# Kernel tuning notes

Hardware: AMD Instinct MI355X
Metric: run time of the kernel (lower is better)

The kernel has to match this reference:

```python
import jax, jax.numpy as jnp
import numpy as np
import math

D_MODEL = 1024
D_HEAD = 64
N_HEADS = D_MODEL // D_HEAD  # 16
COND = 768
EPS = 1e-6


def make_freqs():
    # AxialRoPE(dim=d_head//2, n_heads): freqs linspace in log-space, reshaped [dim//4, nh].T
    dim = D_HEAD // 2  # 32
    n = N_HEADS * dim // 4  # 128
    log_min = math.log(math.pi)
    log_max = math.log(10.0 * math.pi)
    freqs = jnp.exp(jnp.linspace(log_min, log_max, n + 1, dtype=jnp.float32)[:-1])
    return freqs.reshape(dim // 4, N_HEADS).T  # [n_heads, d_head//8] = [16, 8]


def setup_inputs() -> dict:
    key = jax.random.key(0)
    ks = jax.random.split(key, 6)
    N, H, W = 8, 32, 32
    x = jax.random.normal(ks[0], (N, H, W, D_MODEL), jnp.float32)
    pos = jax.random.uniform(ks[1], (N, H, W, 2), jnp.float32) * 2.0 - 1.0
    cond = jax.random.normal(ks[2], (N, COND), jnp.float32)
    norm_w = jax.random.normal(ks[3], (D_MODEL, COND), jnp.float32) * 0.02
    qkv_w = jax.random.normal(ks[4], (3 * D_MODEL, D_MODEL), jnp.float32) / math.sqrt(D_MODEL)
    out_w = jax.random.normal(ks[5], (D_MODEL, D_MODEL), jnp.float32) * 0.02
    scale = jnp.full((N_HEADS,), 10.0, jnp.float32)
    return {"x": x, "pos": pos, "cond": cond, "norm_w": norm_w,
            "qkv_w": qkv_w, "out_w": out_w, "scale": scale}


def rms_norm(x, scale, eps):
    mean_sq = jnp.mean(x * x, axis=-1, keepdims=True)
    return x * (scale * jax.lax.rsqrt(mean_sq + eps))


def apply_rotary(x, theta):
    # rotate first 2*d dims of the head; rest passes through
    d = theta.shape[-1]
    x1, x2, rest = x[..., :d], x[..., d:2 * d], x[..., 2 * d:]
    cos, sin = jnp.cos(theta), jnp.sin(theta)
    return jnp.concatenate([x1 * cos - x2 * sin, x2 * cos + x1 * sin, rest], axis=-1)


def reference(x, pos, cond, norm_w, qkv_w, out_w, scale):
    N, H, W, _ = x.shape
    S = H * W
    skip = x
    # AdaRMSNorm: scale = zero-init linear(cond) + 1
    ns = cond @ norm_w.T  # [N, d_model]
    xn = rms_norm(x, ns[:, None, None, :] + 1.0, EPS)
    # QKV projection, split 'n h w (t nh e)'
    qkv = (xn @ qkv_w.T).reshape(N, S, 3, N_HEADS, D_HEAD)
    q = jnp.transpose(qkv[:, :, 0], (0, 2, 1, 3))  # [N, nh, S, e]
    k = jnp.transpose(qkv[:, :, 1], (0, 2, 1, 3))
    v = jnp.transpose(qkv[:, :, 2], (0, 2, 1, 3))
    # cosine-sim scaling: per-head learned scale, L2-normalize q,k
    sqrt_scale = jnp.sqrt(scale)[:, None, None]  # [nh,1,1]
    q = q * (sqrt_scale * jax.lax.rsqrt(jnp.sum(q * q, -1, keepdims=True) + EPS))
    k = k * (sqrt_scale * jax.lax.rsqrt(jnp.sum(k * k, -1, keepdims=True) + EPS))
    # axial RoPE theta
    freqs = make_freqs()  # [nh, d_head//8]
    pos_f = pos.reshape(N, S, 2)
    theta_h = pos_f[:, :, None, 0:1] * freqs  # [N,S,nh,8]
    theta_w = pos_f[:, :, None, 1:2] * freqs
    theta = jnp.concatenate([theta_h, theta_w], axis=-1)  # [N,S,nh,16]
    theta = jnp.transpose(theta, (0, 2, 1, 3))  # [N,nh,S,16]
    q = apply_rotary(q, theta)
    k = apply_rotary(k, theta)
    # attention with scale=1.0 (cosine-sim already scaled)
    scores = jnp.einsum('bhqe,bhke->bhqk', q, k)
    probs = jax.nn.softmax(scores, axis=-1)
    o = jnp.einsum('bhqk,bhke->bhqe', probs, v)  # [N,nh,S,e]
    o = jnp.transpose(o, (0, 2, 1, 3)).reshape(N, H, W, D_MODEL)
    return o @ out_w.T + skip
```

## Files before the change

kernel.cpp:

```cpp
#include <hip/hip_runtime.h>
#include <hip/hip_bf16.h>
#include <math.h>

typedef __bf16 bf16;
typedef __bf16 bf16x8 __attribute__((ext_vector_type(8)));
typedef __bf16 bf16x4 __attribute__((ext_vector_type(4)));
typedef float f32x4 __attribute__((ext_vector_type(4)));
typedef float f32x16 __attribute__((ext_vector_type(16)));

#define MFMA16(a, b, c) __builtin_amdgcn_mfma_f32_16x16x32_bf16((a), (b), (c), 0, 0, 0)
#define MFMA32(a, b, c) __builtin_amdgcn_mfma_f32_32x32x16_bf16((a), (b), (c), 0, 0, 0)

__device__ __forceinline__ void gload_lds16(const void* g, void* l) {
  __builtin_amdgcn_global_load_lds((__attribute__((address_space(1))) void*)(g),
                                   (__attribute__((address_space(3))) void*)(l),
                                   16, 0, 0);
}

__global__ __launch_bounds__(256) void f2bf_kernel(const float* __restrict__ in0,
                                                   bf16* __restrict__ out0,
                                                   const float* __restrict__ in1,
                                                   bf16* __restrict__ out1, int n0) {
  int i = blockIdx.x * 256 + threadIdx.x;
  const float* in = (i < n0) ? in0 : in1;
  bf16* out = (i < n0) ? out0 : out1;
  int j = (i < n0) ? i : i - n0;
  float4 v = ((const float4*)in)[j];
  bf16x4 o;
  o[0] = (bf16)v.x; o[1] = (bf16)v.y; o[2] = (bf16)v.z; o[3] = (bf16)v.w;
  *(bf16x4*)(out + (size_t)j * 4) = o;
}

__global__ __launch_bounds__(256) void ns_kernel(const float* __restrict__ cond,
                                                 const float* __restrict__ norm_w,
                                                 float* __restrict__ nsp1) {
  int tid = blockIdx.x * 256 + threadIdx.x;
  int b = tid >> 10, c = tid & 1023;
  const float4* wv = (const float4*)(norm_w + (size_t)c * 768);
  const float4* cv = (const float4*)(cond + (size_t)b * 768);
  float acc = 0.f;
#pragma unroll 8
  for (int i = 0; i < 192; ++i) {
    float4 w4 = wv[i], c4 = cv[i];
    acc += w4.x * c4.x + w4.y * c4.y + w4.z * c4.z + w4.w * c4.w;
  }
  nsp1[tid] = acc + 1.0f;
}

__global__ __launch_bounds__(256) void rmsnorm_kernel(const float* __restrict__ x,
                                                      const float* __restrict__ nsp1,
                                                      bf16* __restrict__ xn) {
  int lane = threadIdx.x & 63, w = threadIdx.x >> 6;
  int m = blockIdx.x * 4 + w;
  int b = m >> 10;
  const float* xp = x + (size_t)m * 1024 + lane * 16;
  float v[16];
  float ss = 0.f;
#pragma unroll
  for (int i = 0; i < 4; ++i) {
    float4 t4 = ((const float4*)xp)[i];
    v[4 * i + 0] = t4.x; v[4 * i + 1] = t4.y; v[4 * i + 2] = t4.z; v[4 * i + 3] = t4.w;
    ss += t4.x * t4.x + t4.y * t4.y + t4.z * t4.z + t4.w * t4.w;
  }
#pragma unroll
  for (int off = 32; off >= 1; off >>= 1) ss += __shfl_xor(ss, off);
  float r = rsqrtf(ss * (1.0f / 1024.0f) + 1e-6f);
  const float* np = nsp1 + (size_t)b * 1024 + lane * 16;
  bf16x8 o0, o1;
#pragma unroll
  for (int j = 0; j < 8; ++j) o0[j] = (bf16)(v[j] * np[j] * r);
#pragma unroll
  for (int j = 0; j < 8; ++j) o1[j] = (bf16)(v[8 + j] * np[8 + j] * r);
  bf16* op = xn + (size_t)m * 1024 + lane * 16;
  *(bf16x8*)op = o0;
  *(bf16x8*)(op + 8) = o1;
}

template <int MODE>
__global__ __launch_bounds__(512, 2) void gemm256b(const bf16* __restrict__ A,
                                                   const bf16* __restrict__ B, int nbn,
                                                   bf16* __restrict__ qout, bf16* __restrict__ kout,
                                                   bf16* __restrict__ vtout, float* __restrict__ fout,
                                                   const float* __restrict__ skip,
                                                   const float* __restrict__ pos,
                                                   const float* __restrict__ scale) {
  constexpr int K = 1024;
  __shared__ __align__(16) bf16 sm[36864];
  const int t = threadIdx.x;
  const int cpx = gridDim.x >> 3;
  const int bid = blockIdx.x;
  const int virt = (bid & 7) * cpx + (bid >> 3);
  const int bn = virt % nbn, bm = virt / nbn;
  const int m0 = bm * 256, n0 = bn * 128;
  const int lane = t & 63, wid = t >> 6;
  const int wr = wid >> 1, wc = wid & 1;
  const int r16 = lane & 15, hi = lane >> 4;

  const int tq = t >> 3, c8 = t & 7, cp = c8 ^ (tq & 7);
  const size_t gA = (size_t)(m0 + tq * 2 + (cp >> 2)) * K + (cp & 3) * 8;
  const size_t gB = (size_t)(n0 + tq * 2 + (cp >> 2)) * K + (cp & 3) * 8;
  const size_t gj = (size_t)128 * K;
  const int ldst = t * 8;

  const int chunk = ((r16 & 1) * 4 + hi) ^ (r16 >> 1);
  int aoff[4], boff[4];
#pragma unroll
  for (int fr = 0; fr < 4; ++fr) aoff[fr] = (wr * 32 + fr * 8 + (r16 >> 1)) * 64 + chunk * 8;
#pragma unroll
  for (int fc = 0; fc < 4; ++fc)
    boff[fc] = (wc * 32 + fc * 8 + (r16 >> 1)) * 64 + chunk * 8 + 8192;

  f32x4 acc[4][4] = {};
  constexpr int NS = K >> 5;

#define STG(tile, slot)                                              \
  {                                                                  \
    const bf16* as_ = A + gA + (size_t)(tile) * 32;                  \
    const bf16* bs_ = B + gB + (size_t)(tile) * 32;                  \
    gload_lds16(as_, &sm[(slot) * 12288 + ldst]);                    \
    gload_lds16(as_ + gj, &sm[(slot) * 12288 + 4096 + ldst]);        \
    gload_lds16(bs_, &sm[(slot) * 12288 + 8192 + ldst]);             \
  }

  STG(0, 0);
  STG(1, 1);

  int sl = 0;
  int sl2 = 2;
  for (int s = 0; s < NS; ++s) {
    if (s < NS - 1) {
      asm volatile("s_waitcnt vmcnt(3)" ::: "memory");
    } else {
      asm volatile("s_waitcnt vmcnt(0)" ::: "memory");
    }
    __builtin_amdgcn_s_barrier();
    __builtin_amdgcn_sched_barrier(0);
    if (s + 2 < NS) STG(s + 2, sl2);
    bf16x8 af[4], bfr[4];
    const bf16* base = &sm[sl * 12288];
#pragma unroll
    for (int fr = 0; fr < 4; ++fr) af[fr] = *(const bf16x8*)&base[aoff[fr]];
#pragma unroll
    for (int fc = 0; fc < 4; ++fc) bfr[fc] = *(const bf16x8*)&base[boff[fc]];
    __builtin_amdgcn_s_setprio(1);
#pragma unroll
    for (int fc = 0; fc < 4; ++fc)
#pragma unroll
      for (int fr = 0; fr < 4; ++fr) acc[fr][fc] = MFMA16(af[fr], bfr[fc], acc[fr][fc]);
    __builtin_amdgcn_s_setprio(0);
    sl = (sl == 2) ? 0 : sl + 1;
    sl2 = (sl2 == 2) ? 0 : sl2 + 1;
  }
#undef STG

  if constexpr (MODE == 0) {
    const int p = n0 >> 10;
    if (p == 2) {
      const int hiq = ((hi & 1) << 1) | (hi >> 1);
#pragma unroll
      for (int fr = 0; fr < 4; ++fr) {
        int mrow = m0 + wr * 64 + fr * 16 + hiq * 4;
        int b = mrow >> 10, s0 = mrow & 1023;
#pragma unroll
        for (int fc = 0; fc < 4; ++fc) {
          int n = n0 + wc * 64 + fc * 16 + r16;
          int d = n & 63, hh = (n >> 6) & 15;
          bf16x4 pk;
          pk[0] = (bf16)acc[fr][fc][0]; pk[1] = (bf16)acc[fr][fc][1];
          pk[2] = (bf16)acc[fr][fc][2]; pk[3] = (bf16)acc[fr][fc][3];
          *(bf16x4*)&vtout[(((size_t)(b * 16 + hh) * 64 + d) << 10) + s0] = pk;
        }
      }
    } else {
      const int hh = ((n0 + wc * 64) >> 6) & 15;
      const float LOG2E = 1.4426950408889634f;
      const float sqv = sqrtf(scale[hh]) * (p == 0 ? LOG2E : 1.0f);
      const float f = __expf(1.14472988584940017f +
                             0.0179897502011134460f * (float)((r16 & 7) * 16 + hh));
      const bool is_h = (r16 < 8);
      bf16* dst = (p == 0) ? qout : kout;
#pragma unroll
      for (int fr = 0; fr < 4; ++fr) {
        int mrow = m0 + wr * 64 + fr * 16 + hi * 4;
        int b = mrow >> 10, s0 = mrow & 1023;
        float rr[4];
#pragma unroll
        for (int r = 0; r < 4; ++r) {
          float ss = acc[fr][0][r] * acc[fr][0][r] + acc[fr][1][r] * acc[fr][1][r] +
                     acc[fr][2][r] * acc[fr][2][r] + acc[fr][3][r] * acc[fr][3][r];
          ss += __shfl_xor(ss, 1);
          ss += __shfl_xor(ss, 2);
          ss += __shfl_xor(ss, 4);
          ss += __shfl_xor(ss, 8);
          rr[r] = sqv * rsqrtf(ss + 1e-6f);
        }
#pragma unroll
        for (int r = 0; r < 4; ++r) {
          float2 pp = *(const float2*)&pos[(((size_t)b << 10) + s0 + r) * 2];
          float th = (is_h ? pp.x : pp.y) * f;
          float sv, cv;
          __sincosf(th, &sv, &cv);
          float x1 = acc[fr][0][r] * rr[r];
          float x2 = acc[fr][1][r] * rr[r];
          size_t rowb = (((size_t)(b * 16 + hh) << 10) + s0 + r) * 64;
          dst[rowb + r16]      = (bf16)(x1 * cv - x2 * sv);
          dst[rowb + 16 + r16] = (bf16)(x2 * cv + x1 * sv);
          dst[rowb + 32 + r16] = (bf16)(acc[fr][2][r] * rr[r]);
          dst[rowb + 48 + r16] = (bf16)(acc[fr][3][r] * rr[r]);
        }
      }
    }
  } else {
#pragma unroll
    for (int fr = 0; fr < 4; ++fr) {
      int mrow = m0 + wr * 64 + fr * 16 + hi * 4;
#pragma unroll
      for (int fc = 0; fc < 4; ++fc) {
        int n = n0 + wc * 64 + fc * 16 + r16;
#pragma unroll
        for (int r = 0; r < 4; ++r) {
          size_t off = (size_t)(mrow + r) * 1024 + n;
          fout[off] = acc[fr][fc][r] + skip[off];
        }
      }
    }
  }
}

__global__ __launch_bounds__(256, 4) void attn_kernel(const bf16* __restrict__ q,
                                                      const bf16* __restrict__ k,
                                                      const bf16* __restrict__ vt,
                                                      bf16* __restrict__ o) {
  int bid = blockIdx.x;
  int virt = (bid & 7) * 128 + (bid >> 3);
  const int bh = virt >> 3;
  const int qt = virt & 7;
  const int b = bh >> 4, h = bh & 15;
  const int t = threadIdx.x, lane = t & 63, w = t >> 6;
  const int l31 = lane & 31, h2 = lane >> 5;

  __shared__ bf16 lK[2][4096];
  __shared__ bf16 lV[2][4096];

  const bf16* kp = k + (size_t)bh * 65536;
  const bf16* vp = vt + (size_t)bh * 65536;

  const bf16* qp = q + ((size_t)bh * 1024 + qt * 128 + w * 32) * 64;
  bf16x8 qf[4];
#pragma unroll
  for (int df = 0; df < 4; ++df)
    qf[df] = *(const bf16x8*)&qp[l31 * 64 + df * 16 + h2 * 8];

  bf16x8 ones;
#pragma unroll
  for (int i = 0; i < 8; ++i) ones[i] = (bf16)1.0f;

  const int srow0 = t >> 3, sc0 = t & 7;

  f32x16 oacc0 = {}, oacc1 = {}, lacc = {};

#define STGA(kt_, buf_)                                                            \
  {                                                                                \
    const bf16* kb_ = kp + (kt_) * 4096;                                           \
    const bf16* vb_ = vp + (kt_) * 64;                                             \
    _Pragma("unroll") for (int j = 0; j < 2; ++j) {                                \
      int row = srow0 + j * 32;                                                    \
      int se = ((sc0 ^ (row & 7)) << 3);                                           \
      gload_lds16(kb_ + (size_t)row * 64 + se, &lK[buf_][t * 8 + j * 2048]);       \
      gload_lds16(vb_ + (size_t)row * 1024 + se, &lV[buf_][t * 8 + j * 2048]);     \
    }                                                                              \
  }

  STGA(0, 0);
  STGA(1, 1);

  for (int kt = 0; kt < 16; ++kt) {
    const int cur = kt & 1;
    if (kt < 15) {
      asm volatile("s_waitcnt vmcnt(4)" ::: "memory");
    } else {
      asm volatile("s_waitcnt vmcnt(0)" ::: "memory");
    }
    __builtin_amdgcn_s_barrier();
    __builtin_amdgcn_sched_barrier(0);
    f32x16 sa0 = {}, sa1 = {};
    __builtin_amdgcn_s_setprio(1);
#pragma unroll
    for (int df = 0; df < 4; ++df) {
      int sw = l31 & 7;
      int ce = (((2 * df + h2) ^ sw) << 3);
      bf16x8 kf0 = *(const bf16x8*)&lK[cur][l31 * 64 + ce];
      bf16x8 kf1 = *(const bf16x8*)&lK[cur][(32 + l31) * 64 + ce];
      sa0 = MFMA32(kf0, qf[df], sa0);
      sa1 = MFMA32(kf1, qf[df], sa1);
    }
    __builtin_amdgcn_s_setprio(0);
    bf16x8 pa[4];
#pragma unroll
    for (int e = 0; e < 8; ++e) {
      pa[0][e] = (bf16)exp2f(sa0[e]);
      pa[1][e] = (bf16)exp2f(sa0[e + 8]);
      pa[2][e] = (bf16)exp2f(sa1[e]);
      pa[3][e] = (bf16)exp2f(sa1[e + 8]);
    }
    __builtin_amdgcn_s_setprio(1);
#pragma unroll
    for (int pk = 0; pk < 4; ++pk) {
      lacc = MFMA32(pa[pk], ones, lacc);
#pragma unroll
      for (int db = 0; db < 2; ++db) {
        int row = db * 32 + l31, sw = row & 7;
        bf16x8 vf = *(const bf16x8*)&lV[cur][row * 64 + (((2 * pk + h2) ^ sw) << 3)];
        if (db == 0) oacc0 = MFMA32(pa[pk], vf, oacc0);
        else         oacc1 = MFMA32(pa[pk], vf, oacc1);
      }
    }
    __builtin_amdgcn_s_setprio(0);
    __builtin_amdgcn_sched_barrier(0);
    __builtin_amdgcn_s_barrier();
    __builtin_amdgcn_sched_barrier(0);
    if (kt < 14) STGA(kt + 2, cur);
  }
#undef STGA

  f32x16 inv;
#pragma unroll
  for (int r = 0; r < 16; ++r) inv[r] = 1.f / lacc[r];
#pragma unroll
  for (int r = 0; r < 16; ++r) {
    int qrow = qt * 128 + w * 32 + (r & 3) + 8 * (r >> 2) + 4 * h2;
    size_t rowb = ((size_t)b * 1024 + qrow) * 1024 + h * 64;
    o[rowb + l31]      = (bf16)(oacc0[r] * inv[r]);
    o[rowb + 32 + l31] = (bf16)(oacc1[r] * inv[r]);
  }
}

extern "C" void kernel_launch(void* const* d_in, const int* in_sizes, int n_in,
                              void* d_out, int out_size, void* d_ws, size_t ws_size,
                              hipStream_t stream) {
  const float* x      = (const float*)d_in[0];
  const float* pos    = (const float*)d_in[1];
  const float* cond   = (const float*)d_in[2];
  const float* norm_w = (const float*)d_in[3];
  const float* qkv_w  = (const float*)d_in[4];
  const float* out_w  = (const float*)d_in[5];
  const float* scale  = (const float*)d_in[6];
  float* out = (float*)d_out;

  char* ws = (char*)d_ws;
  bf16* xn        = (bf16*)(ws + 0);
  bf16* qkv_w_bf  = (bf16*)(ws + 16777216);
  bf16* out_w_bf  = (bf16*)(ws + 23068672);
  float* nsp1     = (float*)(ws + 25165824);
  bf16* qraw      = (bf16*)(ws + 25198592);
  bf16* kraw      = (bf16*)(ws + 41975808);
  bf16* vt        = (bf16*)(ws + 58753024);
  bf16* o_attn    = xn;

  f2bf_kernel<<<4096, 256, 0, stream>>>(qkv_w, qkv_w_bf, out_w, out_w_bf, 786432);
  ns_kernel<<<32, 256, 0, stream>>>(cond, norm_w, nsp1);
  rmsnorm_kernel<<<2048, 256, 0, stream>>>(x, nsp1, xn);
  gemm256b<0><<<768, 512, 0, stream>>>(xn, qkv_w_bf, 24, qraw, kraw, vt, nullptr, nullptr,
                                       pos, scale);
  attn_kernel<<<1024, 256, 0, stream>>>(qraw, kraw, vt, o_attn);
  gemm256b<1><<<256, 512, 0, stream>>>(o_attn, out_w_bf, 8, nullptr, nullptr, nullptr, out, x,
                                       nullptr, nullptr);
}
```

Baseline: 187.0 us.

## Add dedicated QKV GEMM with K=64 tiles and split-phase load/MFMA pipeline

Replaces the templated QKV GEMM with a new kernel that stages 64-wide K tiles (16 iterations instead of 32) using a larger 3-slot LDS buffer. Each iteration is split into two phases, and the global-to-LDS loads for the next tile are interleaved between the MFMA halves with extra barriers. The aim is to halve the number of barrier and wait steps and to overlap memory traffic with compute. The larger shared memory footprint (about 144KB per block) may limit occupancy, and the extra barriers add synchronisation. The output projection GEMM becomes a non-templated kernel that keeps only its residual-add epilogue.

```diff
diff --git a/kernel.cpp b/kernel.cpp
--- a/kernel.cpp
+++ b/kernel.cpp
@@ -76,14 +76,180 @@
   *(bf16x8*)(op + 8) = o1;
 }
 
-template <int MODE>
+__global__ __launch_bounds__(512, 2) void gemm8p(const bf16* __restrict__ A,
+                                                 const bf16* __restrict__ B, int nbn,
+                                                 bf16* __restrict__ qout, bf16* __restrict__ kout,
+                                                 bf16* __restrict__ vtout,
+                                                 const float* __restrict__ pos,
+                                                 const float* __restrict__ scale) {
+  constexpr int K = 1024;
+  __shared__ __align__(16) bf16 sm[73728];
+  const int t = threadIdx.x;
+  const int cpx = gridDim.x >> 3;
+  const int bid = blockIdx.x;
+  const int virt = (bid & 7) * cpx + (bid >> 3);
+  const int bn = virt % nbn, bm = virt / nbn;
+  const int m0 = bm * 256, n0 = bn * 128;
+  const int lane = t & 63, wid = t >> 6;
+  const int wr = wid >> 1, wc = wid & 1;
+  const int r16 = lane & 15, hi = lane >> 4;
+  const int sw = r16 & 7;
+
+  const int row0 = t >> 3;
+  const int gc = (t & 7) ^ (row0 & 7);
+  const bf16* gAb = A + (size_t)(m0 + row0) * K + gc * 8;
+  const bf16* gBb = B + (size_t)(n0 + row0) * K + gc * 8;
+  const size_t rstep = (size_t)64 * K;
+  const int ldst = t * 8;
+
+  int aoff2[4][2], boff2[4][2];
+#pragma unroll
+  for (int fr = 0; fr < 4; ++fr)
+#pragma unroll
+    for (int ks = 0; ks < 2; ++ks) {
+      aoff2[fr][ks] = (wr * 64 + fr * 16 + r16) * 64 + (((ks * 4 + hi) ^ sw) << 3);
+      boff2[fr][ks] = 16384 + (wc * 64 + fr * 16 + r16) * 64 + (((ks * 4 + hi) ^ sw) << 3);
+    }
+
+  f32x4 acc[4][4] = {};
+
+#define STG2(tile_, slot_, pr_)                                                       \
+  {                                                                                   \
+    if ((pr_) < 2) {                                                                  \
+      gload_lds16(gAb + rstep * (2 * (pr_)) + (size_t)(tile_) * 64,                   \
+                  &sm[(slot_) * 24576 + (2 * (pr_)) * 4096 + ldst]);                  \
+      gload_lds16(gAb + rstep * (2 * (pr_) + 1) + (size_t)(tile_) * 64,               \
+                  &sm[(slot_) * 24576 + (2 * (pr_) + 1) * 4096 + ldst]);              \
+    } else {                                                                          \
+      gload_lds16(gBb + (size_t)(tile_) * 64, &sm[(slot_) * 24576 + 16384 + ldst]);   \
+      gload_lds16(gBb + rstep + (size_t)(tile_) * 64,                                 \
+                  &sm[(slot_) * 24576 + 20480 + ldst]);                               \
+    }                                                                                 \
+  }
+
+  STG2(0, 0, 0); STG2(0, 0, 1); STG2(0, 0, 2);
+  STG2(1, 1, 0); STG2(1, 1, 1); STG2(1, 1, 2);
+
+  int sl = 0, sl2 = 2;
+  for (int s = 0; s < 16; ++s) {
+    if (s < 15) {
+      asm volatile("s_waitcnt vmcnt(6)" ::: "memory");
+    } else {
+      asm volatile("s_waitcnt vmcnt(0)" ::: "memory");
+    }
+    __builtin_amdgcn_s_barrier();
+    __builtin_amdgcn_sched_barrier(0);
+    const bf16* base = &sm[sl * 24576];
+    const bool st = (s + 2 < 16);
+    bf16x8 ball[4][2], a2[2][2];
+#pragma unroll
+    for (int fc = 0; fc < 4; ++fc)
+#pragma unroll
+      for (int ks = 0; ks < 2; ++ks) ball[fc][ks] = *(const bf16x8*)&base[boff2[fc][ks]];
+#pragma unroll
+    for (int i = 0; i < 2; ++i)
+#pragma unroll
+      for (int ks = 0; ks < 2; ++ks) a2[i][ks] = *(const bf16x8*)&base[aoff2[i][ks]];
+    if (st) { STG2(s + 2, sl2, 0); STG2(s + 2, sl2, 1); }
+    asm volatile("s_waitcnt lgkmcnt(0)" ::: "memory");
+    __builtin_amdgcn_sched_barrier(0);
+    __builtin_amdgcn_s_setprio(1);
+#pragma unroll
+    for (int ks = 0; ks < 2; ++ks)
+#pragma unroll
+      for (int fc = 0; fc < 4; ++fc)
+#pragma unroll
+        for (int i = 0; i < 2; ++i)
+          acc[i][fc] = MFMA16(a2[i][ks], ball[fc][ks], acc[i][fc]);
+    __builtin_amdgcn_s_setprio(0);
+    __builtin_amdgcn_sched_barrier(0);
+    __builtin_amdgcn_s_barrier();
+    bf16x8 a3[2][2];
+#pragma unroll
+    for (int i = 0; i < 2; ++i)
+#pragma unroll
+      for (int ks = 0; ks < 2; ++ks) a3[i][ks] = *(const bf16x8*)&base[aoff2[2 + i][ks]];
+    if (st) STG2(s + 2, sl2, 2);
+    asm volatile("s_waitcnt lgkmcnt(0)" ::: "memory");
+    __builtin_amdgcn_sched_barrier(0);
+    __builtin_amdgcn_s_setprio(1);
+#pragma unroll
+    for (int ks = 0; ks < 2; ++ks)
+#pragma unroll
+      for (int fc = 0; fc < 4; ++fc)
+#pragma unroll
+        for (int i = 0; i < 2; ++i)
+          acc[2 + i][fc] = MFMA16(a3[i][ks], ball[fc][ks], acc[2 + i][fc]);
+    __builtin_amdgcn_s_setprio(0);
+    __builtin_amdgcn_sched_barrier(0);
+    __builtin_amdgcn_s_barrier();
+    sl = (sl == 2) ? 0 : sl + 1;
+    sl2 = (sl2 == 2) ? 0 : sl2 + 1;
+  }
+#undef STG2
+
+  const int p = n0 >> 10;
+  if (p == 2) {
+    const int hiq = ((hi & 1) << 1) | (hi >> 1);
+#pragma unroll
+    for (int fr = 0; fr < 4; ++fr) {
+      int mrow = m0 + wr * 64 + fr * 16 + hiq * 4;
+      int b = mrow >> 10, s0 = mrow & 1023;
+#pragma unroll
+      for (int fc = 0; fc < 4; ++fc) {
+        int n = n0 + wc * 64 + fc * 16 + r16;
+        int d = n & 63, hh = (n >> 6) & 15;
+        bf16x4 pk;
+        pk[0] = (bf16)acc[fr][fc][0]; pk[1] = (bf16)acc[fr][fc][1];
+        pk[2] = (bf16)acc[fr][fc][2]; pk[3] = (bf16)acc[fr][fc][3];
+        *(bf16x4*)&vtout[(((size_t)(b * 16 + hh) * 64 + d) << 10) + s0] = pk;
+      }
+    }
+  } else {
+    const int hh = ((n0 + wc * 64) >> 6) & 15;
+    const float LOG2E = 1.4426950408889634f;
+    const float sqv = sqrtf(scale[hh]) * (p == 0 ? LOG2E : 1.0f);
+    const float f = __expf(1.14472988584940017f +
+                           0.0179897502011134460f * (float)((r16 & 7) * 16 + hh));
+    const bool is_h = (r16 < 8);
+    bf16* dst = (p == 0) ? qout : kout;
+#pragma unroll
+    for (int fr = 0; fr < 4; ++fr) {
+      int mrow = m0 + wr * 64 + fr * 16 + hi * 4;
+      int b = mrow >> 10, s0 = mrow & 1023;
+      float rr[4];
+#pragma unroll
+      for (int r = 0; r < 4; ++r) {
+        float ss = acc[fr][0][r] * acc[fr][0][r] + acc[fr][1][r] * acc[fr][1][r] +
+                   acc[fr][2][r] * acc[fr][2][r] + acc[fr][3][r] * acc[fr][3][r];
+        ss += __shfl_xor(ss, 1);
+        ss += __shfl_xor(ss, 2);
+        ss += __shfl_xor(ss, 4);
+        ss += __shfl_xor(ss, 8);
+        rr[r] = sqv * rsqrtf(ss + 1e-6f);
+      }
+#pragma unroll
+      for (int r = 0; r < 4; ++r) {
+        float2 pp = *(const float2*)&pos[(((size_t)b << 10) + s0 + r) * 2];
+        float th = (is_h ? pp.x : pp.y) * f;
+        float sv, cv;
+        __sincosf(th, &sv, &cv);
+        float x1 = acc[fr][0][r] * rr[r];
+        float x2 = acc[fr][1][r] * rr[r];
+        size_t rowb = (((size_t)(b * 16 + hh) << 10) + s0 + r) * 64;
+        dst[rowb + r16]      = (bf16)(x1 * cv - x2 * sv);
+        dst[rowb + 16 + r16] = (bf16)(x2 * cv + x1 * sv);
+        dst[rowb + 32 + r16] = (bf16)(acc[fr][2][r] * rr[r]);
+        dst[rowb + 48 + r16] = (bf16)(acc[fr][3][r] * rr[r]);
+      }
+    }
+  }
+}
+
 __global__ __launch_bounds__(512, 2) void gemm256b(const bf16* __restrict__ A,
                                                    const bf16* __restrict__ B, int nbn,
-                                                   bf16* __restrict__ qout, bf16* __restrict__ kout,
-                                                   bf16* __restrict__ vtout, float* __restrict__ fout,
-                                                   const float* __restrict__ skip,
-                                                   const float* __restrict__ pos,
-                                                   const float* __restrict__ scale) {
+                                                   float* __restrict__ fout,
+                                                   const float* __restrict__ skip) {
   constexpr int K = 1024;
   __shared__ __align__(16) bf16 sm[36864];
   const int t = threadIdx.x;
@@ -125,8 +291,7 @@
   STG(0, 0);
   STG(1, 1);
 
-  int sl = 0;
-  int sl2 = 2;
+  int sl = 0, sl2 = 2;
   for (int s = 0; s < NS; ++s) {
     if (s < NS - 1) {
       asm volatile("s_waitcnt vmcnt(3)" ::: "memory");
@@ -153,75 +318,16 @@
   }
 #undef STG
 
-  if constexpr (MODE == 0) {
-    const int p = n0 >> 10;
-    if (p == 2) {
-      const int hiq = ((hi & 1) << 1) | (hi >> 1);
-#pragma unroll
-      for (int fr = 0; fr < 4; ++fr) {
-        int mrow = m0 + wr * 64 + fr * 16 + hiq * 4;
-        int b = mrow >> 10, s0 = mrow & 1023;
-#pragma unroll
-        for (int fc = 0; fc < 4; ++fc) {
-          int n = n0 + wc * 64 + fc * 16 + r16;
-          int d = n & 63, hh = (n >> 6) & 15;
-          bf16x4 pk;
-          pk[0] = (bf16)acc[fr][fc][0]; pk[1] = (bf16)acc[fr][fc][1];
-          pk[2] = (bf16)acc[fr][fc][2]; pk[3] = (bf16)acc[fr][fc][3];
-          *(bf16x4*)&vtout[(((size_t)(b * 16 + hh) * 64 + d) << 10) + s0] = pk;
-        }
-      }
-    } else {
-      const int hh = ((n0 + wc * 64) >> 6) & 15;
-      const float LOG2E = 1.4426950408889634f;
-      const float sqv = sqrtf(scale[hh]) * (p == 0 ? LOG2E : 1.0f);
-      const float f = __expf(1.14472988584940017f +
-                             0.0179897502011134460f * (float)((r16 & 7) * 16 + hh));
-      const bool is_h = (r16 < 8);
-      bf16* dst = (p == 0) ? qout : kout;
-#pragma unroll
-      for (int fr = 0; fr < 4; ++fr) {
-        int mrow = m0 + wr * 64 + fr * 16 + hi * 4;
-        int b = mrow >> 10, s0 = mrow & 1023;
-        float rr[4];
-#pragma unroll
-        for (int r = 0; r < 4; ++r) {
-          float ss = acc[fr][0][r] * acc[fr][0][r] + acc[fr][1][r] * acc[fr][1][r] +
-                     acc[fr][2][r] * acc[fr][2][r] + acc[fr][3][r] * acc[fr][3][r];
-          ss += __shfl_xor(ss, 1);
-          ss += __shfl_xor(ss, 2);
-          ss += __shfl_xor(ss, 4);
-          ss += __shfl_xor(ss, 8);
-          rr[r] = sqv * rsqrtf(ss + 1e-6f);
-        }
-#pragma unroll
-        for (int r = 0; r < 4; ++r) {
-          float2 pp = *(const float2*)&pos[(((size_t)b << 10) + s0 + r) * 2];
-          float th = (is_h ? pp.x : pp.y) * f;
-          float sv, cv;
-          __sincosf(th, &sv, &cv);
-          float x1 = acc[fr][0][r] * rr[r];
-          float x2 = acc[fr][1][r] * rr[r];
-          size_t rowb = (((size_t)(b * 16 + hh) << 10) + s0 + r) * 64;
-          dst[rowb + r16]      = (bf16)(x1 * cv - x2 * sv);
-          dst[rowb + 16 + r16] = (bf16)(x2 * cv + x1 * sv);
-          dst[rowb + 32 + r16] = (bf16)(acc[fr][2][r] * rr[r]);
-          dst[rowb + 48 + r16] = (bf16)(acc[fr][3][r] * rr[r]);
-        }
-      }
-    }
-  } else {
-#pragma unroll
-    for (int fr = 0; fr < 4; ++fr) {
-      int mrow = m0 + wr * 64 + fr * 16 + hi * 4;
-#pragma unroll
-      for (int fc = 0; fc < 4; ++fc) {
-        int n = n0 + wc * 64 + fc * 16 + r16;
-#pragma unroll
-        for (int r = 0; r < 4; ++r) {
-          size_t off = (size_t)(mrow + r) * 1024 + n;
-          fout[off] = acc[fr][fc][r] + skip[off];
-        }
+#pragma unroll
+  for (int fr = 0; fr < 4; ++fr) {
+    int mrow = m0 + wr * 64 + fr * 16 + hi * 4;
+#pragma unroll
+    for (int fc = 0; fc < 4; ++fc) {
+      int n = n0 + wc * 64 + fc * 16 + r16;
+#pragma unroll
+      for (int r = 0; r < 4; ++r) {
+        size_t off = (size_t)(mrow + r) * 1024 + n;
+        fout[off] = acc[fr][fc][r] + skip[off];
       }
     }
   }
@@ -360,9 +466,7 @@
   f2bf_kernel<<<4096, 256, 0, stream>>>(qkv_w, qkv_w_bf, out_w, out_w_bf, 786432);
   ns_kernel<<<32, 256, 0, stream>>>(cond, norm_w, nsp1);
   rmsnorm_kernel<<<2048, 256, 0, stream>>>(x, nsp1, xn);
-  gemm256b<0><<<768, 512, 0, stream>>>(xn, qkv_w_bf, 24, qraw, kraw, vt, nullptr, nullptr,
-                                       pos, scale);
+  gemm8p<<<768, 512, 0, stream>>>(xn, qkv_w_bf, 24, qraw, kraw, vt, pos, scale);
   attn_kernel<<<1024, 256, 0, stream>>>(qraw, kraw, vt, o_attn);
-  gemm256b<1><<<256, 512, 0, stream>>>(o_attn, out_w_bf, 8, nullptr, nullptr, nullptr, out, x,
-                                       nullptr, nullptr);
-}
+  gemm256b<<<256, 512, 0, stream>>>(o_attn, out_w_bf, 8, out, x);
+}
```

Result: no change. 185.7 us, median of 2 (-0.7%).

## Pre-swizzle QKV weights into fragment layout and load B directly to registers

Applied to the files above, without the earlier changes.

QKV weights are now converted to bf16 and rearranged into an MFMA-fragment-ordered flat layout, so the QKV GEMM can load B operands straight from global memory into registers with double buffering. Only A goes through LDS. This cuts shared memory per block enough to allow 4 blocks per CU instead of 2. The trade-off is more register pressure and direct global loads for B that no longer share staging across waves, and the out-projection GEMM is split into its own non-templated kernel.

```diff
diff --git a/kernel.cpp b/kernel.cpp
--- a/kernel.cpp
+++ b/kernel.cpp
@@ -17,18 +17,25 @@
                                    16, 0, 0);
 }
 
-__global__ __launch_bounds__(256) void f2bf_kernel(const float* __restrict__ in0,
-                                                   bf16* __restrict__ out0,
-                                                   const float* __restrict__ in1,
-                                                   bf16* __restrict__ out1, int n0) {
+__global__ __launch_bounds__(256) void qkvrepack_kernel(const float* __restrict__ in,
+                                                        bf16* __restrict__ outf) {
   int i = blockIdx.x * 256 + threadIdx.x;
-  const float* in = (i < n0) ? in0 : in1;
-  bf16* out = (i < n0) ? out0 : out1;
-  int j = (i < n0) ? i : i - n0;
-  float4 v = ((const float4*)in)[j];
+  int n = i >> 8, k = (i & 255) * 4;
+  float4 v = *(const float4*)&in[(size_t)n * 1024 + k];
   bf16x4 o;
   o[0] = (bf16)v.x; o[1] = (bf16)v.y; o[2] = (bf16)v.z; o[3] = (bf16)v.w;
-  *(bf16x4*)(out + (size_t)j * 4) = o;
+  size_t flat = (size_t)((n >> 7) * 32 + (k >> 5)) * 4096 + ((n >> 6) & 1) * 2048 +
+                ((n >> 4) & 3) * 512 + ((k >> 3) & 3) * 128 + (n & 15) * 8 + (k & 7);
+  *(bf16x4*)&outf[flat] = o;
+}
+
+__global__ __launch_bounds__(256) void f2bf_kernel(const float* __restrict__ in,
+                                                   bf16* __restrict__ out) {
+  int i = blockIdx.x * 256 + threadIdx.x;
+  float4 v = ((const float4*)in)[i];
+  bf16x4 o;
+  o[0] = (bf16)v.x; o[1] = (bf16)v.y; o[2] = (bf16)v.z; o[3] = (bf16)v.w;
+  *(bf16x4*)(out + (size_t)i * 4) = o;
 }
 
 __global__ __launch_bounds__(256) void ns_kernel(const float* __restrict__ cond,
@@ -76,14 +83,143 @@
   *(bf16x8*)(op + 8) = o1;
 }
 
-template <int MODE>
+__global__ __launch_bounds__(512, 4) void gemmflat(const bf16* __restrict__ A,
+                                                   const bf16* __restrict__ Bflat, int nbn,
+                                                   bf16* __restrict__ qout, bf16* __restrict__ kout,
+                                                   bf16* __restrict__ vtout,
+                                                   const float* __restrict__ pos,
+                                                   const float* __restrict__ scale) {
+  constexpr int K = 1024;
+  __shared__ __align__(16) bf16 sm[24576];
+  const int t = threadIdx.x;
+  const int cpx = gridDim.x >> 3;
+  const int bid = blockIdx.x;
+  const int virt = (bid & 7) * cpx + (bid >> 3);
+  const int nb = virt % nbn, bm = virt / nbn;
+  const int m0 = bm * 256, n0 = nb * 128;
+  const int lane = t & 63, wid = t >> 6;
+  const int wr = wid >> 1, wc = wid & 1;
+  const int r16 = lane & 15, hi = lane >> 4;
+
+  const int tq = t >> 3, c8 = t & 7, cp = c8 ^ (tq & 7);
+  const size_t gA = (size_t)(m0 + tq * 2 + (cp >> 2)) * K + (cp & 3) * 8;
+  const size_t gj = (size_t)128 * K;
+  const int ldst = t * 8;
+
+  const int chunk = ((r16 & 1) * 4 + hi) ^ (r16 >> 1);
+  int aoff[4];
+#pragma unroll
+  for (int fr = 0; fr < 4; ++fr) aoff[fr] = (wr * 32 + fr * 8 + (r16 >> 1)) * 64 + chunk * 8;
+
+  const bf16* bfp = Bflat + (size_t)nb * 131072 + wc * 2048 + lane * 8;
+
+  f32x4 acc[4][4] = {};
+  bf16x8 bbuf[2][4];
+
+#define STGA(tile_, slot_)                                             \
+  {                                                                    \
+    const bf16* as_ = A + gA + (size_t)(tile_) * 32;                   \
+    gload_lds16(as_, &sm[(slot_) * 8192 + ldst]);                      \
+    gload_lds16(as_ + gj, &sm[(slot_) * 8192 + 4096 + ldst]);          \
+  }
+
+  STGA(0, 0);
+#pragma unroll
+  for (int fc = 0; fc < 4; ++fc) bbuf[0][fc] = *(const bf16x8*)(bfp + fc * 512);
+  STGA(1, 1);
+
+#pragma unroll
+  for (int s = 0; s < 32; ++s) {
+    if (s < 31) {
+      asm volatile("s_waitcnt vmcnt(2)" ::: "memory");
+    } else {
+      asm volatile("s_waitcnt vmcnt(0)" ::: "memory");
+    }
+    __builtin_amdgcn_s_barrier();
+    __builtin_amdgcn_sched_barrier(0);
+    if (s + 1 < 32) {
+#pragma unroll
+      for (int fc = 0; fc < 4; ++fc)
+        bbuf[(s + 1) & 1][fc] = *(const bf16x8*)(bfp + (s + 1) * 4096 + fc * 512);
+    }
+    if (s + 2 < 32) STGA(s + 2, (s + 2) % 3);
+    __builtin_amdgcn_sched_barrier(0);
+    bf16x8 af[4];
+    const bf16* base = &sm[(s % 3) * 8192];
+#pragma unroll
+    for (int fr = 0; fr < 4; ++fr) af[fr] = *(const bf16x8*)&base[aoff[fr]];
+    __builtin_amdgcn_s_setprio(1);
+#pragma unroll
+    for (int fc = 0; fc < 4; ++fc)
+#pragma unroll
+      for (int fr = 0; fr < 4; ++fr) acc[fr][fc] = MFMA16(af[fr], bbuf[s & 1][fc], acc[fr][fc]);
+    __builtin_amdgcn_s_setprio(0);
+    __builtin_amdgcn_sched_barrier(0);
+  }
+#undef STGA
+
+  const int p = n0 >> 10;
+  if (p == 2) {
+    const int hiq = ((hi & 1) << 1) | (hi >> 1);
+#pragma unroll
+    for (int fr = 0; fr < 4; ++fr) {
+      int mrow = m0 + wr * 64 + fr * 16 + hiq * 4;
+      int b = mrow >> 10, s0 = mrow & 1023;
+#pragma unroll
+      for (int fc = 0; fc < 4; ++fc) {
+        int n = n0 + wc * 64 + fc * 16 + r16;
+        int d = n & 63, hh = (n >> 6) & 15;
+        bf16x4 pk;
+        pk[0] = (bf16)acc[fr][fc][0]; pk[1] = (bf16)acc[fr][fc][1];
+        pk[2] = (bf16)acc[fr][fc][2]; pk[3] = (bf16)acc[fr][fc][3];
+        *(bf16x4*)&vtout[(((size_t)(b * 16 + hh) * 64 + d) << 10) + s0] = pk;
+      }
+    }
+  } else {
+    const int hh = ((n0 + wc * 64) >> 6) & 15;
+    const float LOG2E = 1.4426950408889634f;
+    const float sqv = sqrtf(scale[hh]) * (p == 0 ? LOG2E : 1.0f);
+    const float f = __expf(1.14472988584940017f +
+                           0.0179897502011134460f * (float)((r16 & 7) * 16 + hh));
+    const bool is_h = (r16 < 8);
+    bf16* dst = (p == 0) ? qout : kout;
+#pragma unroll
+    for (int fr = 0; fr < 4; ++fr) {
+      int mrow = m0 + wr * 64 + fr * 16 + hi * 4;
+      int b = mrow >> 10, s0 = mrow & 1023;
+      float rr[4];
+#pragma unroll
+      for (int r = 0; r < 4; ++r) {
+        float ss = acc[fr][0][r] * acc[fr][0][r] + acc[fr][1][r] * acc[fr][1][r] +
+                   acc[fr][2][r] * acc[fr][2][r] + acc[fr][3][r] * acc[fr][3][r];
+        ss += __shfl_xor(ss, 1);
+        ss += __shfl_xor(ss, 2);
+        ss += __shfl_xor(ss, 4);
+        ss += __shfl_xor(ss, 8);
+        rr[r] = sqv * rsqrtf(ss + 1e-6f);
+      }
+#pragma unroll
+      for (int r = 0; r < 4; ++r) {
+        float2 pp = *(const float2*)&pos[(((size_t)b << 10) + s0 + r) * 2];
+        float th = (is_h ? pp.x : pp.y) * f;
+        float sv, cv;
+        __sincosf(th, &sv, &cv);
+        float x1 = acc[fr][0][r] * rr[r];
+        float x2 = acc[fr][1][r] * rr[r];
+        size_t rowb = (((size_t)(b * 16 + hh) << 10) + s0 + r) * 64;
+        dst[rowb + r16]      = (bf16)(x1 * cv - x2 * sv);
+        dst[rowb + 16 + r16] = (bf16)(x2 * cv + x1 * sv);
+        dst[rowb + 32 + r16] = (bf16)(acc[fr][2][r] * rr[r]);
+        dst[rowb + 48 + r16] = (bf16)(acc[fr][3][r] * rr[r]);
+      }
+    }
+  }
+}
+
 __global__ __launch_bounds__(512, 2) void gemm256b(const bf16* __restrict__ A,
                                                    const bf16* __restrict__ B, int nbn,
-                                                   bf16* __restrict__ qout, bf16* __restrict__ kout,
-                                                   bf16* __restrict__ vtout, float* __restrict__ fout,
-                                                   const float* __restrict__ skip,
-                                                   const float* __restrict__ pos,
-                                                   const float* __restrict__ scale) {
+                                                   float* __restrict__ fout,
+                                                   const float* __restrict__ skip) {
   constexpr int K = 1024;
   __shared__ __align__(16) bf16 sm[36864];
   const int t = threadIdx.x;
@@ -125,8 +261,7 @@
   STG(0, 0);
   STG(1, 1);
 
-  int sl = 0;
-  int sl2 = 2;
+  int sl = 0, sl2 = 2;
   for (int s = 0; s < NS; ++s) {
     if (s < NS - 1) {
       asm volatile("s_waitcnt vmcnt(3)" ::: "memory");
@@ -153,75 +288,16 @@
   }
 #undef STG
 
-  if constexpr (MODE == 0) {
-    const int p = n0 >> 10;
-    if (p == 2) {
-      const int hiq = ((hi & 1) << 1) | (hi >> 1);
-#pragma unroll
-      for (int fr = 0; fr < 4; ++fr) {
-        int mrow = m0 + wr * 64 + fr * 16 + hiq * 4;
-        int b = mrow >> 10, s0 = mrow & 1023;
-#pragma unroll
-        for (int fc = 0; fc < 4; ++fc) {
-          int n = n0 + wc * 64 + fc * 16 + r16;
-          int d = n & 63, hh = (n >> 6) & 15;
-          bf16x4 pk;
-          pk[0] = (bf16)acc[fr][fc][0]; pk[1] = (bf16)acc[fr][fc][1];
-          pk[2] = (bf16)acc[fr][fc][2]; pk[3] = (bf16)acc[fr][fc][3];
-          *(bf16x4*)&vtout[(((size_t)(b * 16 + hh) * 64 + d) << 10) + s0] = pk;
-        }
-      }
-    } else {
-      const int hh = ((n0 + wc * 64) >> 6) & 15;
-      const float LOG2E = 1.4426950408889634f;
-      const float sqv = sqrtf(scale[hh]) * (p == 0 ? LOG2E : 1.0f);
-      const float f = __expf(1.14472988584940017f +
-                             0.0179897502011134460f * (float)((r16 & 7) * 16 + hh));
-      const bool is_h = (r16 < 8);
-      bf16* dst = (p == 0) ? qout : kout;
-#pragma unroll
-      for (int fr = 0; fr < 4; ++fr) {
-        int mrow = m0 + wr * 64 + fr * 16 + hi * 4;
-        int b = mrow >> 10, s0 = mrow & 1023;
-        float rr[4];
-#pragma unroll
-        for (int r = 0; r < 4; ++r) {
-          float ss = acc[fr][0][r] * acc[fr][0][r] + acc[fr][1][r] * acc[fr][1][r] +
-                     acc[fr][2][r] * acc[fr][2][r] + acc[fr][3][r] * acc[fr][3][r];
-          ss += __shfl_xor(ss, 1);
-          ss += __shfl_xor(ss, 2);
-          ss += __shfl_xor(ss, 4);
-          ss += __shfl_xor(ss, 8);
-          rr[r] = sqv * rsqrtf(ss + 1e-6f);
-        }
-#pragma unroll
-        for (int r = 0; r < 4; ++r) {
-          float2 pp = *(const float2*)&pos[(((size_t)b << 10) + s0 + r) * 2];
-          float th = (is_h ? pp.x : pp.y) * f;
-          float sv, cv;
-          __sincosf(th, &sv, &cv);
-          float x1 = acc[fr][0][r] * rr[r];
-          float x2 = acc[fr][1][r] * rr[r];
-          size_t rowb = (((size_t)(b * 16 + hh) << 10) + s0 + r) * 64;
-          dst[rowb + r16]      = (bf16)(x1 * cv - x2 * sv);
-          dst[rowb + 16 + r16] = (bf16)(x2 * cv + x1 * sv);
-          dst[rowb + 32 + r16] = (bf16)(acc[fr][2][r] * rr[r]);
-          dst[rowb + 48 + r16] = (bf16)(acc[fr][3][r] * rr[r]);
-        }
-      }
-    }
-  } else {
-#pragma unroll
-    for (int fr = 0; fr < 4; ++fr) {
-      int mrow = m0 + wr * 64 + fr * 16 + hi * 4;
-#pragma unroll
-      for (int fc = 0; fc < 4; ++fc) {
-        int n = n0 + wc * 64 + fc * 16 + r16;
-#pragma unroll
-        for (int r = 0; r < 4; ++r) {
-          size_t off = (size_t)(mrow + r) * 1024 + n;
-          fout[off] = acc[fr][fc][r] + skip[off];
-        }
+#pragma unroll
+  for (int fr = 0; fr < 4; ++fr) {
+    int mrow = m0 + wr * 64 + fr * 16 + hi * 4;
+#pragma unroll
+    for (int fc = 0; fc < 4; ++fc) {
+      int n = n0 + wc * 64 + fc * 16 + r16;
+#pragma unroll
+      for (int r = 0; r < 4; ++r) {
+        size_t off = (size_t)(mrow + r) * 1024 + n;
+        fout[off] = acc[fr][fc][r] + skip[off];
       }
     }
   }
@@ -349,7 +425,7 @@
 
   char* ws = (char*)d_ws;
   bf16* xn        = (bf16*)(ws + 0);
-  bf16* qkv_w_bf  = (bf16*)(ws + 16777216);
+  bf16* Bflat     = (bf16*)(ws + 16777216);
   bf16* out_w_bf  = (bf16*)(ws + 23068672);
   float* nsp1     = (float*)(ws + 25165824);
   bf16* qraw      = (bf16*)(ws + 25198592);
@@ -357,12 +433,11 @@
   bf16* vt        = (bf16*)(ws + 58753024);
   bf16* o_attn    = xn;
 
-  f2bf_kernel<<<4096, 256, 0, stream>>>(qkv_w, qkv_w_bf, out_w, out_w_bf, 786432);
+  qkvrepack_kernel<<<3072, 256, 0, stream>>>(qkv_w, Bflat);
+  f2bf_kernel<<<1024, 256, 0, stream>>>(out_w, out_w_bf);
   ns_kernel<<<32, 256, 0, stream>>>(cond, norm_w, nsp1);
   rmsnorm_kernel<<<2048, 256, 0, stream>>>(x, nsp1, xn);
-  gemm256b<0><<<768, 512, 0, stream>>>(xn, qkv_w_bf, 24, qraw, kraw, vt, nullptr, nullptr,
-                                       pos, scale);
+  gemmflat<<<768, 512, 0, stream>>>(xn, Bflat, 24, qraw, kraw, vt, pos, scale);
   attn_kernel<<<1024, 256, 0, stream>>>(qraw, kraw, vt, o_attn);
-  gemm256b<1><<<256, 512, 0, stream>>>(o_attn, out_w_bf, 8, nullptr, nullptr, nullptr, out, x,
-                                       nullptr, nullptr);
-}
+  gemm256b<<<256, 512, 0, stream>>>(o_attn, out_w_bf, 8, out, x);
+}
```

Result: slower. 198.1 us (+6.0%).
